# Kernel tuning notes

Measured on AMD Instinct MI355X. Metric: run time of the kernel, lower is better.

Reference implementation:

```python
import jax, jax.numpy as jnp
import numpy as np
from jax import lax

# dims per init_kwargs
Y_CH = 8        # y_channels
N    = 16       # trial_num (batch)
L    = 4096     # trial_length
C    = 16       # channel_kernel_num
K    = 64       # kernel_size
T    = 10       # e_opt_iterations (FISTA steps)
LIP  = 10.0     # smoothness_param (Lipschitz constant)
LAM  = 0.1      # e_reg_coeff (l1 penalty)


def _conv1d(x, Hk):
    # analysis operator H^T: x [N, Cin, Lx], Hk [Cout, Cin, K] -> [N, Cout, Lx-K+1]
    # (cross-correlation, VALID padding, matches torch.nn.functional.conv1d)
    return lax.conv_general_dilated(x, Hk, (1,), 'VALID',
                                    dimension_numbers=('NCH', 'OIH', 'NCH'))


def _conv_transpose1d(x, Hk):
    # synthesis operator H: x [N, C, enc], Hk [C, 1, K] -> [N, 1, enc+K-1]
    # torch conv_transpose1d == conv with swapped io channels, flipped kernel, FULL pad
    Ht = jnp.flip(jnp.swapaxes(Hk, 0, 1), -1)  # [1, C, K]
    return lax.conv_general_dilated(x, Ht, (1,), [(K - 1, K - 1)],
                                    dimension_numbers=('NCH', 'OIH', 'NCH'))


def _fista_encode(y_c, H_c):
    # y_c: [N, 1, L] single-electrode trials; H_c: [C, 1, K] kernels for this channel
    enc_dim = y_c.shape[-1] - K + 1
    x0 = jnp.zeros((y_c.shape[0], C, enc_dim), y_c.dtype)

    def step(carry, _):
        x_old, x_tmp, s_old = carry
        res = y_c - _conv_transpose1d(x_tmp, H_c)          # reconstruction residual
        x_new = jax.nn.relu(x_tmp + _conv1d(res, H_c) / LIP - LAM / LIP)
        s_new = (1.0 + jnp.sqrt(1.0 + 4.0 * s_old * s_old)) / 2.0
        x_tmp_new = x_new + (s_old - 1.0) / s_new * (x_new - x_old)
        return (x_new, x_tmp_new, s_new), None

    (x_new, _, _), _ = lax.scan(step, (x0, x0, jnp.float32(1.0)), None, length=T)
    return x_new  # [N, C, enc_dim]


def setup_inputs() -> dict:
    key = jax.random.key(0)
    k1, k2 = jax.random.split(key)
    y = jax.random.normal(k1, (N, Y_CH, L), dtype=jnp.float32)
    # one dictionary per recorded channel: H_{c} params, shape [C, 1, K]
    H = jax.random.normal(k2, (Y_CH, C, 1, K), dtype=jnp.float32) * 0.1
    return {"y": y, "H": H}


def reference(y, H):
    # y: [N, Y_CH, L]; H: [Y_CH, C, 1, K]
    ys = jnp.swapaxes(y, 0, 1)[:, :, None, :]   # [Y_CH, N, 1, L]
    # independent FISTA sparse-coding per electrode channel
    return jax.vmap(_fista_encode)(ys, H)        # [Y_CH, N, C, L-K+1]
```

## Files before the change

kernel.cpp:

```cpp
#include <hip/hip_runtime.h>
#include <cmath>

#define YCH 8
#define NTR 16
#define LLEN 4096
#define CK  16
#define KS  64
#define ENC 4033
#define NP  128
#define INV_LIP 0.1f
#define THRESH 0.01f

#define XW4 272
#define XP4 289
#define SW(s) ((s) + ((s) >> 4))

typedef float vfloat4 __attribute__((ext_vector_type(4)));

__device__ __forceinline__ vfloat4 ldvol(const vfloat4* p) {
    return *(const volatile vfloat4*)p;
}

#define C4(v, c) ((c) == 0 ? (v).x : (c) == 1 ? (v).y : (c) == 2 ? (v).z : (v).w)
#define GW(f) ((f) < 4  ? C4(w0, (f))      : \
               (f) < 8  ? C4(w1, (f) - 4)  : \
               (f) < 12 ? C4(w2, (f) - 8)  : \
               (f) < 16 ? C4(w3, (f) - 12) : C4(w4, (f) - 16))

__device__ __forceinline__ float4 loadB4(const float* __restrict__ A,
                                         const float* __restrict__ P,
                                         float gamma, size_t coff, int gi4)
{
    if (gi4 >= 0 && gi4 + 3 < ENC) {
        float4 a = *(const float4*)(A + coff + gi4);
        float4 p = *(const float4*)(P + coff + gi4);
        return make_float4(fmaf(gamma, a.x - p.x, a.x),
                           fmaf(gamma, a.y - p.y, a.y),
                           fmaf(gamma, a.z - p.z, a.z),
                           fmaf(gamma, a.w - p.w, a.w));
    }
    float r[4];
    #pragma unroll
    for (int j = 0; j < 4; ++j) {
        int gi = gi4 + j;
        if (gi >= 0 && gi < ENC) {
            float a = A[coff + gi], p = P[coff + gi];
            r[j] = fmaf(gamma, a - p, a);
        } else r[j] = 0.f;
    }
    return make_float4(r[0], r[1], r[2], r[3]);
}

__global__ __launch_bounds__(256) void resid_quad(
    const float* __restrict__ H,
    const float* __restrict__ Acur, const float* __restrict__ Aprev,
    float gamma, float* __restrict__ part)
{
    __shared__ __align__(16) float xs[4 * XP4 * 4];
    __shared__ __align__(16) float hs[4 * KS];
    const int tid = threadIdx.x;
    const int t0  = blockIdx.x * 1024;
    const int c0  = blockIdx.y * 4;
    const int p   = blockIdx.z;
    const int ch  = p >> 4;

    if (tid < 64)
        ((float4*)hs)[tid] = ((const float4*)(H + ((size_t)ch * CK + c0) * KS))[tid];

    const size_t pbase = (size_t)p * CK * ENC;
    #pragma unroll
    for (int s = 0; s < 5; ++s) {
        int l4 = tid + 256 * s;
        if (l4 < 4 * XW4) {
            int c   = l4 / XW4;
            int off = l4 - c * XW4;
            ((float4*)xs)[c * XP4 + SW(off)] =
                loadB4(Acur, Aprev, gamma,
                       pbase + (size_t)(c0 + c) * ENC, t0 - 64 + 4 * off);
        }
    }
    __syncthreads();

    float acc[4] = {0.f, 0.f, 0.f, 0.f};

    #pragma unroll
    for (int cc = 0; cc < 4; ++cc) {
        const vfloat4* xb = (const vfloat4*)xs + cc * XP4;
        const float4*  hc = (const float4*)(hs + cc * KS);

        vfloat4 w0 = ldvol(xb + SW(tid + 12));
        vfloat4 w1 = ldvol(xb + SW(tid + 13));
        vfloat4 w2 = ldvol(xb + SW(tid + 14));
        vfloat4 w3 = ldvol(xb + SW(tid + 15));
        vfloat4 w4 = ldvol(xb + SW(tid + 16));
        #pragma unroll
        for (int kg = 0; kg < 4; ++kg) {
            const float4 h0 = hc[4 * kg], h1 = hc[4 * kg + 1];
            const float4 h2 = hc[4 * kg + 2], h3 = hc[4 * kg + 3];
            #pragma unroll
            for (int mm = 0; mm < 16; ++mm) {
                const float4 hv = (mm < 4 ? h0 : mm < 8 ? h1 : mm < 12 ? h2 : h3);
                const float hm = ((mm & 3) == 0 ? hv.x : (mm & 3) == 1 ? hv.y :
                                  (mm & 3) == 2 ? hv.z : hv.w);
                #pragma unroll
                for (int j = 0; j < 4; ++j)
                    acc[j] = fmaf(GW(16 - mm + j), hm, acc[j]);
            }
            if (kg < 3) {
                w4 = w0;
                w0 = ldvol(xb + SW(tid + 8  - 4 * kg));
                w1 = ldvol(xb + SW(tid + 9  - 4 * kg));
                w2 = ldvol(xb + SW(tid + 10 - 4 * kg));
                w3 = ldvol(xb + SW(tid + 11 - 4 * kg));
            }
        }
    }

    const int t = t0 + 4 * tid;
    *(float4*)(part + ((size_t)blockIdx.y * NP + p) * LLEN + t) =
        make_float4(acc[0], acc[1], acc[2], acc[3]);
}

__global__ __launch_bounds__(256) void fista_quad(
    const float* __restrict__ y, const float* __restrict__ part,
    const float* __restrict__ H,
    const float* __restrict__ Acur, const float* __restrict__ Aprev,
    float gamma, int first, float* __restrict__ Anext)
{
    __shared__ __align__(16) float rs[XW4 * 4];
    __shared__ __align__(16) float hs[4 * KS];
    const int tid = threadIdx.x;
    const int i0  = blockIdx.x * 1024;
    const int c0  = blockIdx.y * 4;
    const int p   = blockIdx.z;
    const int n = p & 15, ch = p >> 4;

    if (tid < 64)
        ((float4*)hs)[tid] = ((const float4*)(H + ((size_t)ch * CK + c0) * KS))[tid];

    const float* ybase = y + ((size_t)n * YCH + ch) * LLEN;
    #pragma unroll
    for (int s = 0; s < 2; ++s) {
        int l4 = tid + 256 * s;
        if (l4 < XW4) {
            int gi4 = i0 + 4 * l4;
            float4 v;
            if (gi4 + 3 < LLEN) {
                v = *(const float4*)(ybase + gi4);
                if (!first) {
                    #pragma unroll
                    for (int q = 0; q < 4; ++q) {
                        float4 pv = *(const float4*)(part + ((size_t)q * NP + p) * LLEN + gi4);
                        v.x -= pv.x; v.y -= pv.y; v.z -= pv.z; v.w -= pv.w;
                    }
                }
            } else {
                float r[4];
                #pragma unroll
                for (int j = 0; j < 4; ++j) {
                    int gi = gi4 + j;
                    if (gi < LLEN) {
                        float t = ybase[gi];
                        if (!first) {
                            #pragma unroll
                            for (int q = 0; q < 4; ++q)
                                t -= part[((size_t)q * NP + p) * LLEN + gi];
                        }
                        r[j] = t;
                    } else r[j] = 0.f;
                }
                v = make_float4(r[0], r[1], r[2], r[3]);
            }
            ((float4*)rs)[l4] = v;
        }
    }
    __syncthreads();

    float wf[68];
    const float4* rr = (const float4*)rs + tid;
    #pragma unroll
    for (int q = 0; q < 17; ++q) {
        float4 t4 = rr[q];
        wf[4*q] = t4.x; wf[4*q+1] = t4.y; wf[4*q+2] = t4.z; wf[4*q+3] = t4.w;
    }

    const int i = i0 + 4 * tid;
    const size_t pb = (size_t)p * CK * ENC;
    const bool vec = (i + 3 < ENC);

    float4 a0 = make_float4(0,0,0,0), p0 = make_float4(0,0,0,0);
    if (!first && vec) {
        a0 = *(const float4*)(Acur  + pb + (size_t)c0 * ENC + i);
        p0 = *(const float4*)(Aprev + pb + (size_t)c0 * ENC + i);
    }

    for (int cc = 0; cc < 4; ++cc) {
        float4 a1 = make_float4(0,0,0,0), p1 = make_float4(0,0,0,0);
        if (!first && vec && cc < 3) {
            a1 = *(const float4*)(Acur  + pb + (size_t)(c0 + cc + 1) * ENC + i);
            p1 = *(const float4*)(Aprev + pb + (size_t)(c0 + cc + 1) * ENC + i);
        }

        float acc[4] = {0.f, 0.f, 0.f, 0.f};
        const float4* hc = (const float4*)(hs + cc * KS);
        #pragma unroll
        for (int g = 0; g < 16; ++g) {
            float4 h4 = hc[g];
            float hh[4] = {h4.x, h4.y, h4.z, h4.w};
            #pragma unroll
            for (int m = 0; m < 4; ++m) {
                const int k = 4 * g + m;
                #pragma unroll
                for (int j = 0; j < 4; ++j)
                    acc[j] = fmaf(wf[k + j], hh[m], acc[j]);
            }
        }

        const size_t idx = pb + (size_t)(c0 + cc) * ENC + i;
        if (vec) {
            float B[4] = {0.f, 0.f, 0.f, 0.f};
            if (!first) {
                float av[4] = {a0.x, a0.y, a0.z, a0.w};
                float pv[4] = {p0.x, p0.y, p0.z, p0.w};
                #pragma unroll
                for (int j = 0; j < 4; ++j) B[j] = fmaf(gamma, av[j] - pv[j], av[j]);
            }
            float4 o;
            o.x = fmaxf(fmaf(acc[0], INV_LIP, B[0]) - THRESH, 0.f);
            o.y = fmaxf(fmaf(acc[1], INV_LIP, B[1]) - THRESH, 0.f);
            o.z = fmaxf(fmaf(acc[2], INV_LIP, B[2]) - THRESH, 0.f);
            o.w = fmaxf(fmaf(acc[3], INV_LIP, B[3]) - THRESH, 0.f);
            *(float4*)(Anext + idx) = o;
        } else if (i < ENC) {
            #pragma unroll
            for (int j = 0; j < 4; ++j) {
                if (i + j < ENC) {
                    float B = 0.f;
                    if (!first) {
                        float a = Acur[idx + j], pp = Aprev[idx + j];
                        B = fmaf(gamma, a - pp, a);
                    }
                    Anext[idx + j] = fmaxf(fmaf(acc[j], INV_LIP, B) - THRESH, 0.f);
                }
            }
        }
        a0 = a1; p0 = p1;
    }
}

extern "C" void kernel_launch(void* const* d_in, const int* in_sizes, int n_in,
                              void* d_out, int out_size, void* d_ws, size_t ws_size,
                              hipStream_t stream)
{
    const float* y = (const float*)d_in[0];
    const float* H = (const float*)d_in[1];
    const size_t XSZ = (size_t)NP * CK * ENC;

    float* bufA = (float*)d_ws;
    float* bufB = (float*)d_out;
    float* part = bufA + XSZ;

    double s[11]; s[0] = 1.0;
    for (int t = 1; t <= 10; ++t) s[t] = 0.5 * (1.0 + sqrt(1.0 + 4.0 * s[t-1] * s[t-1]));

    dim3 gR(4, 4, NP), gF(4, 4, NP);

    for (int t = 0; t < 10; ++t) {
        float gamma = (t == 0) ? 0.f : (float)((s[t-1] - 1.0) / s[t]);
        float* Anext       = (t & 1) ? bufB : bufA;
        const float* Acur  = (t & 1) ? bufA : bufB;
        const float* Aprev = (t <= 1) ? Acur
                                      : ((t & 1) ? bufB : bufA);
        if (t == 0) {
            fista_quad<<<gF, 256, 0, stream>>>(y, part, H, bufA, bufA, 0.f, 1, bufA);
        } else {
            resid_quad<<<gR, 256, 0, stream>>>(H, Acur, Aprev, gamma, part);
            fista_quad<<<gF, 256, 0, stream>>>(y, part, H, Acur, Aprev, gamma, 0, Anext);
        }
    }
}
```

Before: 491.9 us.

## Synthesize from current iterate only and reuse previous synthesis via linearity

The synthesis kernel now convolves only the current iterate instead of the momentum-extrapolated one. The residual is rebuilt as y − (1+γ)·H·x_cur + γ·H·x_prev, with the previous synthesis kept in a double-buffered workspace. This drops the extra load of the previous iterate in the synthesis pass. Each block now covers 8 channels, so 2 partial sums are written instead of 4, which shrinks the partial-sum traffic read by the FISTA kernel. The cost is more shared memory per block and fewer blocks, and the fused kernel reads two partial-sum pairs once momentum is active.

```diff
diff --git a/kernel.cpp b/kernel.cpp
--- a/kernel.cpp
+++ b/kernel.cpp
@@ -22,61 +22,48 @@
 }
 
 #define C4(v, c) ((c) == 0 ? (v).x : (c) == 1 ? (v).y : (c) == 2 ? (v).z : (v).w)
-#define GW(f) ((f) < 4  ? C4(w0, (f))      : \
-               (f) < 8  ? C4(w1, (f) - 4)  : \
-               (f) < 12 ? C4(w2, (f) - 8)  : \
-               (f) < 16 ? C4(w3, (f) - 12) : C4(w4, (f) - 16))
-
-__device__ __forceinline__ float4 loadB4(const float* __restrict__ A,
-                                         const float* __restrict__ P,
-                                         float gamma, size_t coff, int gi4)
-{
-    if (gi4 >= 0 && gi4 + 3 < ENC) {
-        float4 a = *(const float4*)(A + coff + gi4);
-        float4 p = *(const float4*)(P + coff + gi4);
-        return make_float4(fmaf(gamma, a.x - p.x, a.x),
-                           fmaf(gamma, a.y - p.y, a.y),
-                           fmaf(gamma, a.z - p.z, a.z),
-                           fmaf(gamma, a.w - p.w, a.w));
-    }
+#define GW5(f) ((f) < 4  ? C4(w0, (f))      : \
+                (f) < 8  ? C4(w1, (f) - 4)  : \
+                (f) < 12 ? C4(w2, (f) - 8)  : \
+                (f) < 16 ? C4(w3, (f) - 12) : C4(w4, (f) - 16))
+
+__device__ __forceinline__ float4 loadA4(const float* __restrict__ A,
+                                         size_t coff, int gi4)
+{
+    if (gi4 >= 0 && gi4 + 3 < ENC) return *(const float4*)(A + coff + gi4);
     float r[4];
     #pragma unroll
     for (int j = 0; j < 4; ++j) {
         int gi = gi4 + j;
-        if (gi >= 0 && gi < ENC) {
-            float a = A[coff + gi], p = P[coff + gi];
-            r[j] = fmaf(gamma, a - p, a);
-        } else r[j] = 0.f;
+        r[j] = (gi >= 0 && gi < ENC) ? A[coff + gi] : 0.f;
     }
     return make_float4(r[0], r[1], r[2], r[3]);
 }
 
-__global__ __launch_bounds__(256) void resid_quad(
-    const float* __restrict__ H,
-    const float* __restrict__ Acur, const float* __restrict__ Aprev,
-    float gamma, float* __restrict__ part)
-{
-    __shared__ __align__(16) float xs[4 * XP4 * 4];
-    __shared__ __align__(16) float hs[4 * KS];
+__global__ __launch_bounds__(256) void synth_half(
+    const float* __restrict__ H, const float* __restrict__ A,
+    float* __restrict__ S)
+{
+    __shared__ __align__(16) float xs[8 * XP4 * 4];
+    __shared__ __align__(16) float hs[8 * KS];
     const int tid = threadIdx.x;
     const int t0  = blockIdx.x * 1024;
-    const int c0  = blockIdx.y * 4;
+    const int c0  = blockIdx.y * 8;
     const int p   = blockIdx.z;
     const int ch  = p >> 4;
 
-    if (tid < 64)
+    if (tid < 128)
         ((float4*)hs)[tid] = ((const float4*)(H + ((size_t)ch * CK + c0) * KS))[tid];
 
     const size_t pbase = (size_t)p * CK * ENC;
     #pragma unroll
-    for (int s = 0; s < 5; ++s) {
+    for (int s = 0; s < 9; ++s) {
         int l4 = tid + 256 * s;
-        if (l4 < 4 * XW4) {
+        if (l4 < 8 * XW4) {
             int c   = l4 / XW4;
             int off = l4 - c * XW4;
             ((float4*)xs)[c * XP4 + SW(off)] =
-                loadB4(Acur, Aprev, gamma,
-                       pbase + (size_t)(c0 + c) * ENC, t0 - 64 + 4 * off);
+                loadA4(A, pbase + (size_t)(c0 + c) * ENC, t0 - 64 + 4 * off);
         }
     }
     __syncthreads();
@@ -84,7 +71,7 @@
     float acc[4] = {0.f, 0.f, 0.f, 0.f};
 
     #pragma unroll
-    for (int cc = 0; cc < 4; ++cc) {
+    for (int cc = 0; cc < 8; ++cc) {
         const vfloat4* xb = (const vfloat4*)xs + cc * XP4;
         const float4*  hc = (const float4*)(hs + cc * KS);
 
@@ -95,16 +82,15 @@
         vfloat4 w4 = ldvol(xb + SW(tid + 16));
         #pragma unroll
         for (int kg = 0; kg < 4; ++kg) {
-            const float4 h0 = hc[4 * kg], h1 = hc[4 * kg + 1];
-            const float4 h2 = hc[4 * kg + 2], h3 = hc[4 * kg + 3];
+            const float4 h0 = hc[4*kg],   h1 = hc[4*kg+1];
+            const float4 h2 = hc[4*kg+2], h3 = hc[4*kg+3];
             #pragma unroll
             for (int mm = 0; mm < 16; ++mm) {
                 const float4 hv = (mm < 4 ? h0 : mm < 8 ? h1 : mm < 12 ? h2 : h3);
-                const float hm = ((mm & 3) == 0 ? hv.x : (mm & 3) == 1 ? hv.y :
-                                  (mm & 3) == 2 ? hv.z : hv.w);
+                const float hm = C4(hv, mm & 3);
                 #pragma unroll
                 for (int j = 0; j < 4; ++j)
-                    acc[j] = fmaf(GW(16 - mm + j), hm, acc[j]);
+                    acc[j] = fmaf(GW5(16 - mm + j), hm, acc[j]);
             }
             if (kg < 3) {
                 w4 = w0;
@@ -117,15 +103,17 @@
     }
 
     const int t = t0 + 4 * tid;
-    *(float4*)(part + ((size_t)blockIdx.y * NP + p) * LLEN + t) =
+    *(float4*)(S + ((size_t)blockIdx.y * NP + p) * LLEN + t) =
         make_float4(acc[0], acc[1], acc[2], acc[3]);
 }
 
 __global__ __launch_bounds__(256) void fista_quad(
-    const float* __restrict__ y, const float* __restrict__ part,
+    const float* __restrict__ y,
+    const float* __restrict__ Scur, const float* __restrict__ Sprev,
     const float* __restrict__ H,
     const float* __restrict__ Acur, const float* __restrict__ Aprev,
-    float gamma, int first, float* __restrict__ Anext)
+    float gamma, int first, int two, float c1, float c2,
+    float* __restrict__ Anext)
 {
     __shared__ __align__(16) float rs[XW4 * 4];
     __shared__ __align__(16) float hs[4 * KS];
@@ -148,10 +136,15 @@
             if (gi4 + 3 < LLEN) {
                 v = *(const float4*)(ybase + gi4);
                 if (!first) {
-                    #pragma unroll
-                    for (int q = 0; q < 4; ++q) {
-                        float4 pv = *(const float4*)(part + ((size_t)q * NP + p) * LLEN + gi4);
-                        v.x -= pv.x; v.y -= pv.y; v.z -= pv.z; v.w -= pv.w;
+                    float4 a = *(const float4*)(Scur + ((size_t)0 * NP + p) * LLEN + gi4);
+                    float4 b = *(const float4*)(Scur + ((size_t)1 * NP + p) * LLEN + gi4);
+                    v.x -= c1 * (a.x + b.x); v.y -= c1 * (a.y + b.y);
+                    v.z -= c1 * (a.z + b.z); v.w -= c1 * (a.w + b.w);
+                    if (two) {
+                        float4 e = *(const float4*)(Sprev + ((size_t)0 * NP + p) * LLEN + gi4);
+                        float4 f = *(const float4*)(Sprev + ((size_t)1 * NP + p) * LLEN + gi4);
+                        v.x += c2 * (e.x + f.x); v.y += c2 * (e.y + f.y);
+                        v.z += c2 * (e.z + f.z); v.w += c2 * (e.w + f.w);
                     }
                 }
             } else {
@@ -162,9 +155,11 @@
                     if (gi < LLEN) {
                         float t = ybase[gi];
                         if (!first) {
-                            #pragma unroll
-                            for (int q = 0; q < 4; ++q)
-                                t -= part[((size_t)q * NP + p) * LLEN + gi];
+                            t -= c1 * (Scur[((size_t)0 * NP + p) * LLEN + gi] +
+                                       Scur[((size_t)1 * NP + p) * LLEN + gi]);
+                            if (two)
+                                t += c2 * (Sprev[((size_t)0 * NP + p) * LLEN + gi] +
+                                           Sprev[((size_t)1 * NP + p) * LLEN + gi]);
                         }
                         r[j] = t;
                     } else r[j] = 0.f;
@@ -255,15 +250,16 @@
     const float* y = (const float*)d_in[0];
     const float* H = (const float*)d_in[1];
     const size_t XSZ = (size_t)NP * CK * ENC;
+    const size_t RSZ = (size_t)NP * LLEN;
 
     float* bufA = (float*)d_ws;
     float* bufB = (float*)d_out;
-    float* part = bufA + XSZ;
+    float* Sgen = bufA + XSZ;
 
     double s[11]; s[0] = 1.0;
     for (int t = 1; t <= 10; ++t) s[t] = 0.5 * (1.0 + sqrt(1.0 + 4.0 * s[t-1] * s[t-1]));
 
-    dim3 gR(4, 4, NP), gF(4, 4, NP);
+    dim3 gS(4, 2, NP), gF(4, 4, NP);
 
     for (int t = 0; t < 10; ++t) {
         float gamma = (t == 0) ? 0.f : (float)((s[t-1] - 1.0) / s[t]);
@@ -272,10 +268,15 @@
         const float* Aprev = (t <= 1) ? Acur
                                       : ((t & 1) ? bufB : bufA);
         if (t == 0) {
-            fista_quad<<<gF, 256, 0, stream>>>(y, part, H, bufA, bufA, 0.f, 1, bufA);
+            fista_quad<<<gF, 256, 0, stream>>>(y, Sgen, Sgen, H, bufA, bufA,
+                                               0.f, 1, 0, 0.f, 0.f, bufA);
         } else {
-            resid_quad<<<gR, 256, 0, stream>>>(H, Acur, Aprev, gamma, part);
-            fista_quad<<<gF, 256, 0, stream>>>(y, part, H, Acur, Aprev, gamma, 0, Anext);
-        }
-    }
-}
+            float* Sc = Sgen + (size_t)((t - 1) & 1) * 2 * RSZ;
+            float* Sp = Sgen + (size_t)(t & 1) * 2 * RSZ;
+            synth_half<<<gS, 256, 0, stream>>>(H, Acur, Sc);
+            fista_quad<<<gF, 256, 0, stream>>>(y, Sc, Sp, H, Acur, Aprev,
+                                               gamma, 0, (t >= 2) ? 1 : 0,
+                                               1.f + gamma, gamma, Anext);
+        }
+    }
+}
```

Measured after the change: 482.1 us. 2.0% less time.
